# Optimization experiments

Hardware: AMD Instinct MI355X
Metric: run time of the kernel (lower is better)

Reference implementation:

```python
import jax, jax.numpy as jnp
import numpy as np

N = 100000   # total nodes (batched molecules)
E = 250000   # directed edges
B = 2000     # number of graphs
F_IN = 75    # atom feature dim
DIM = 32     # hidden dim


def setup_inputs() -> dict:
    key = jax.random.key(0)
    ks = jax.random.split(key, 12)
    def gl(k, shape, fan_in):
        return (jax.random.normal(k, shape, jnp.float32) / np.sqrt(fan_in)).astype(jnp.float32)
    inp = {}
    inp['node_features'] = jax.random.normal(ks[0], (N, F_IN), jnp.float32)
    inp['edge_features'] = jax.random.normal(ks[1], (E, 11), jnp.float32)
    inp['lin0_w'] = gl(ks[2], (DIM, F_IN), F_IN)
    inp['lin0_b'] = jnp.zeros((DIM,), jnp.float32)
    # edge network: Linear(11,128) -> ReLU -> Linear(128, DIM*DIM)
    inp['nn_w1'] = gl(ks[3], (128, 11), 11)
    inp['nn_b1'] = jnp.zeros((128,), jnp.float32)
    inp['nn_w2'] = gl(ks[4], (DIM * DIM, 128), 128)
    inp['nn_b2'] = jnp.zeros((DIM * DIM,), jnp.float32)
    inp['conv_bias'] = jnp.zeros((DIM,), jnp.float32)  # NNConv bias (root_weight=False)
    # GRU(dim, dim), torch gate order: r, z, n
    inp['gru_wih'] = gl(ks[5], (3 * DIM, DIM), DIM)
    inp['gru_whh'] = gl(ks[6], (3 * DIM, DIM), DIM)
    inp['gru_bih'] = jnp.zeros((3 * DIM,), jnp.float32)
    inp['gru_bhh'] = jnp.zeros((3 * DIM,), jnp.float32)
    # Set2Set LSTM(2*dim, dim), torch gate order: i, f, g, o
    inp['lstm_wih'] = gl(ks[7], (4 * DIM, 2 * DIM), 2 * DIM)
    inp['lstm_whh'] = gl(ks[8], (4 * DIM, DIM), DIM)
    inp['lstm_bih'] = jnp.zeros((4 * DIM,), jnp.float32)
    inp['lstm_bhh'] = jnp.zeros((4 * DIM,), jnp.float32)
    inp['edge_index'] = jax.random.randint(ks[9], (2, E), 0, N)
    inp['graph_index'] = jnp.sort(jax.random.randint(ks[10], (N,), 0, B))
    return inp


def _nnconv(x, edge_w, src, dst, bias):
    # per-edge: gather src features, apply [dim,dim] edge weight, scatter-mean to dst
    msg = jnp.einsum('ei,eio->eo', x[src], edge_w)           # [E, DIM]
    s = jax.ops.segment_sum(msg, dst, num_segments=N)         # [N, DIM]
    cnt = jax.ops.segment_sum(jnp.ones((msg.shape[0],), msg.dtype), dst, num_segments=N)
    mean = s / jnp.maximum(cnt, 1.0)[:, None]
    return mean + bias


def _gru_cell(x, h, wih, whh, bih, bhh):
    gi = x @ wih.T + bih
    gh = h @ whh.T + bhh
    gi_r, gi_z, gi_n = jnp.split(gi, 3, axis=-1)
    gh_r, gh_z, gh_n = jnp.split(gh, 3, axis=-1)
    r = jax.nn.sigmoid(gi_r + gh_r)
    z = jax.nn.sigmoid(gi_z + gh_z)
    n = jnp.tanh(gi_n + r * gh_n)
    return (1.0 - z) * n + z * h


def _lstm_cell(x, h, c, wih, whh, bih, bhh):
    g = x @ wih.T + bih + h @ whh.T + bhh
    i, f, gg, o = jnp.split(g, 4, axis=-1)
    c = jax.nn.sigmoid(f) * c + jax.nn.sigmoid(i) * jnp.tanh(gg)
    h = jax.nn.sigmoid(o) * jnp.tanh(c)
    return h, c


def _set2set(x, batch, wih, whh, bih, bhh, steps=3):
    dim = x.shape[-1]
    h = jnp.zeros((B, dim), x.dtype)
    c = jnp.zeros((B, dim), x.dtype)
    q_star = jnp.zeros((B, 2 * dim), x.dtype)
    for _ in range(steps):
        q, c = _lstm_cell(q_star, h, c, wih, whh, bih, bhh)
        h = q
        e = jnp.sum(x * q[batch], axis=-1)                    # [N]
        emax = jax.ops.segment_max(e, batch, num_segments=B)
        ex = jnp.exp(e - emax[batch])
        denom = jax.ops.segment_sum(ex, batch, num_segments=B)
        a = ex / denom[batch]
        r = jax.ops.segment_sum(a[:, None] * x, batch, num_segments=B)
        q_star = jnp.concatenate([q, r], axis=-1)
    return q_star


def reference(node_features, edge_features, lin0_w, lin0_b, nn_w1, nn_b1, nn_w2, nn_b2,
              conv_bias, gru_wih, gru_whh, gru_bih, gru_bhh,
              lstm_wih, lstm_whh, lstm_bih, lstm_bhh, edge_index, graph_index):
    src, dst = edge_index[0], edge_index[1]
    out = jax.nn.relu(node_features @ lin0_w.T + lin0_b)      # [N, DIM]
    # edge network (edge_features are fixed -> identical every iteration)
    hw = jax.nn.relu(edge_features @ nn_w1.T + nn_b1)
    edge_w = (hw @ nn_w2.T + nn_b2).reshape(-1, DIM, DIM)     # [E, DIM, DIM]
    h = out
    for _ in range(3):
        m = jax.nn.relu(_nnconv(out, edge_w, src, dst, conv_bias))
        h = _gru_cell(m, h, gru_wih, gru_whh, gru_bih, gru_bhh)
        out = h
    pooled = _set2set(out, graph_index, lstm_wih, lstm_whh, lstm_bih, lstm_bhh)
    return pooled, out
```

## Files before the change

kernel.cpp:

```cpp
#include <hip/hip_runtime.h>
#include <stdint.h>

#define N_NODES  100000
#define N_EDGES  250000
#define N_GRAPHS 2000
#define F_IN     75
#define DIM      32
#define H1       128

#define MSG_BLOCKS 977
#define CH        8
#define NSTAGES   17
#define KT_PAD    (CH * NSTAGES)
#define W2F_HALFS (KT_PAD * 1024)

typedef _Float16 v8h __attribute__((ext_vector_type(8)));
typedef float    v4f __attribute__((ext_vector_type(4)));

__device__ __forceinline__ void gld_lds16(const void* g, void* l) {
    __builtin_amdgcn_global_load_lds(
        (const __attribute__((address_space(1))) unsigned int*)g,
        (__attribute__((address_space(3))) unsigned int*)l, 16, 0, 0);
}

__global__ __launch_bounds__(256) void lin0_kernel(
    const float* __restrict__ nf, const float* __restrict__ w,
    const float* __restrict__ b, float* __restrict__ h) {
    __shared__ float wl[DIM * F_IN];
    __shared__ float bl[DIM];
    int t = threadIdx.x;
    for (int i = t; i < DIM * F_IN; i += 256) wl[i] = w[i];
    if (t < DIM) bl[t] = b[t];
    __syncthreads();
    int nl = t >> 5, o = t & 31;
    #pragma unroll
    for (int p = 0; p < 4; ++p) {
        int n = blockIdx.x * 32 + p * 8 + nl;
        if (n >= N_NODES) continue;
        const float* row = nf + (size_t)n * F_IN;
        float acc = bl[o];
        #pragma unroll
        for (int i = 0; i < F_IN; ++i) acc += row[i] * wl[o * F_IN + i];
        h[n * DIM + o] = fmaxf(acc, 0.f);
    }
}

__global__ __launch_bounds__(256) void prep_w2f_kernel(
    const float* __restrict__ w2, const float* __restrict__ b2,
    _Float16* __restrict__ w2f) {
    int id = blockIdx.x * 256 + threadIdx.x;
    if (id >= W2F_HALFS) return;
    int j    = id & 7;
    int lane = (id >> 3) & 63;
    int ng   = (id >> 9) & 1;
    int kt   = id >> 10;
    int lr = lane & 15, q = lane >> 4;
    int c = kt * 32 + q * 8 + j;
    int o = ng * 16 + lr;
    float val = 0.f;
    if (c < 4096)      val = w2[((c >> 7) * 32 + o) * H1 + (c & 127)];
    else if (c < 4128) val = b2[(c - 4096) * 32 + o];
    w2f[id] = (_Float16)val;
}

__global__ __launch_bounds__(256) void hw_kernel(
    const float* __restrict__ ef, const float* __restrict__ w1,
    const float* __restrict__ b1, _Float16* __restrict__ hwf,
    int e_off) {
    __shared__ float wl[H1 * 11];
    __shared__ float bl[H1];
    int t = threadIdx.x;
    for (int i = t; i < H1 * 11; i += 256) wl[i] = w1[i];
    if (t < H1) bl[t] = b1[t];
    __syncthreads();
    int k = t & 127;
    #pragma unroll
    for (int p = 0; p < 16; ++p) {
        int le = blockIdx.x * 32 + p * 2 + (t >> 7);
        int e  = e_off + le;
        float acc = 0.f;
        if (e < N_EDGES) {
            const float* row = ef + (size_t)e * 11;
            acc = bl[k];
            #pragma unroll
            for (int i = 0; i < 11; ++i) acc += row[i] * wl[k * 11 + i];
            acc = fmaxf(acc, 0.f);
        }
        size_t addr = (size_t)(le >> 4) * 2048 + (k >> 3) * 128 + (le & 15) * 8 + (k & 7);
        hwf[addr] = (_Float16)acc;
    }
}

__global__ __launch_bounds__(256) void cnt_kernel(
    const int* __restrict__ dst, float* __restrict__ cnt) {
    int e = blockIdx.x * 256 + threadIdx.x;
    if (e < N_EDGES) atomicAdd(&cnt[dst[e]], 1.0f);
}

__global__ __launch_bounds__(256) void offs_kernel(
    const int* __restrict__ gidx, int* __restrict__ gstart) {
    int n = blockIdx.x * 256 + threadIdx.x;
    if (n >= N_NODES) return;
    int b = gidx[n];
    if (n == 0) {
        for (int bb = 0; bb <= b; ++bb) gstart[bb] = 0;
    } else {
        int a = gidx[n - 1];
        for (int bb = a + 1; bb <= b; ++bb) gstart[bb] = n;
    }
    if (n == N_NODES - 1) {
        for (int bb = b + 1; bb <= N_GRAPHS; ++bb) gstart[bb] = N_NODES;
    }
}

__global__ __launch_bounds__(256) void msg_kernel(
    const _Float16* __restrict__ hwf, const _Float16* __restrict__ w2f,
    const float* __restrict__ x, const int* __restrict__ src,
    const int* __restrict__ dst, float* __restrict__ sbuf, int e_off) {
    __shared__ _Float16 xs[32 * 256];
    __shared__ _Float16 bst[2][CH * 1024];

    int t = threadIdx.x;
    int w = t >> 6, lane = t & 63, lr = lane & 15, q = lane >> 4;
    int wbase = w * 64;

    {
        const char* gp = (const char*)w2f;
        char* lp = (char*)&bst[0][0];
        #pragma unroll
        for (int it = 0; it < 4; ++it)
            gld_lds16(gp + it * 4096 + t * 16, lp + it * 4096 + t * 16);
    }

    v8h hwr[4][4];
    {
        const v8h* hv = (const v8h*)hwf;
        int T0 = blockIdx.x * 16 + w * 4;
        #pragma unroll
        for (int mt = 0; mt < 4; ++mt)
            #pragma unroll
            for (int kc = 0; kc < 4; ++kc)
                hwr[mt][kc] = hv[(size_t)(T0 + mt) * 256 + (kc * 4 + q) * 16 + lr];
    }

    {
        int e = e_off + blockIdx.x * 256 + t;
        int ec = e < N_EDGES ? e : N_EDGES - 1;
        int sv = src[ec];
        const float4* xr = (const float4*)(x + (size_t)sv * DIM);
        #pragma unroll
        for (int u = 0; u < 8; ++u) {
            float4 v = xr[u];
            xs[(u * 4 + 0) * 256 + t] = (_Float16)v.x;
            xs[(u * 4 + 1) * 256 + t] = (_Float16)v.y;
            xs[(u * 4 + 2) * 256 + t] = (_Float16)v.z;
            xs[(u * 4 + 3) * 256 + t] = (_Float16)v.w;
        }
    }
    __syncthreads();

    v4f acc[4][2];
    #pragma unroll
    for (int mt = 0; mt < 4; ++mt)
        #pragma unroll
        for (int ng = 0; ng < 2; ++ng) { v4f z = {0.f, 0.f, 0.f, 0.f}; acc[mt][ng] = z; }

    _Float16 xsc[4];

    for (int s = 0; s < NSTAGES - 1; ++s) {
        {
            const char* gp = (const char*)(w2f + (size_t)(s + 1) * CH * 1024);
            char* lp = (char*)&bst[(s + 1) & 1][0];
            #pragma unroll
            for (int it = 0; it < 4; ++it)
                gld_lds16(gp + it * 4096 + t * 16, lp + it * 4096 + t * 16);
        }
        const _Float16* bb = &bst[s & 1][0];
        #pragma unroll
        for (int ktl = 0; ktl < CH; ++ktl) {
            int kt = s * CH + ktl;
            v8h b0 = *(const v8h*)(bb + ktl * 1024 + lane * 8);
            v8h b1 = *(const v8h*)(bb + ktl * 1024 + 512 + lane * 8);
            if ((kt & 3) == 0) {
                int i = kt >> 2;
                #pragma unroll
                for (int mt = 0; mt < 4; ++mt)
                    xsc[mt] = xs[i * 256 + wbase + mt * 16 + lr];
            }
            int kc = kt & 3;
            #pragma unroll
            for (int mt = 0; mt < 4; ++mt) {
                v8h a = hwr[mt][kc] * xsc[mt];
                acc[mt][0] = __builtin_amdgcn_mfma_f32_16x16x32_f16(a, b0, acc[mt][0], 0, 0, 0);
                acc[mt][1] = __builtin_amdgcn_mfma_f32_16x16x32_f16(a, b1, acc[mt][1], 0, 0, 0);
            }
        }
        __syncthreads();
    }
    {
        const _Float16* bb = &bst[0][0];
        v8h b0 = *(const v8h*)(bb + lane * 8);
        v8h b1 = *(const v8h*)(bb + 512 + lane * 8);
        #pragma unroll
        for (int mt = 0; mt < 4; ++mt) {
            v8h a;
            #pragma unroll
            for (int j = 0; j < 8; ++j)
                a[j] = xs[(q * 8 + j) * 256 + wbase + mt * 16 + lr];
            acc[mt][0] = __builtin_amdgcn_mfma_f32_16x16x32_f16(a, b0, acc[mt][0], 0, 0, 0);
            acc[mt][1] = __builtin_amdgcn_mfma_f32_16x16x32_f16(a, b1, acc[mt][1], 0, 0, 0);
        }
    }

    int E0 = e_off + blockIdx.x * 256 + wbase;
    #pragma unroll
    for (int mt = 0; mt < 4; ++mt) {
        #pragma unroll
        for (int r = 0; r < 4; ++r) {
            int e = E0 + mt * 16 + q * 4 + r;
            if (e < N_EDGES) {
                int dv = dst[e];
                float* sp = sbuf + (size_t)dv * DIM;
                atomicAdd(sp + lr,      acc[mt][0][r]);
                atomicAdd(sp + 16 + lr, acc[mt][1][r]);
            }
        }
    }
}

__global__ __launch_bounds__(256) void gru_kernel(
    const float* __restrict__ s, const float* __restrict__ cnt,
    const float* __restrict__ cb,
    const float* __restrict__ wih, const float* __restrict__ whh,
    const float* __restrict__ bih, const float* __restrict__ bhh,
    float* __restrict__ h) {
    __shared__ _Float16 m_l[64 * 32];
    __shared__ _Float16 h_l[64 * 32];
    int t = threadIdx.x;

    {
        int node_l = t >> 2, part = t & 3;
        int n = blockIdx.x * 64 + node_l;
        int nc = n < N_NODES ? n : N_NODES - 1;
        float c = cnt[nc];
        float rc = 1.f / (c > 1.f ? c : 1.f);
        const float4* s4 = (const float4*)(s + (size_t)nc * DIM + part * 8);
        float4 sa = s4[0], sb = s4[1];
        const float* cbp = cb + part * 8;
        v8h mv;
        mv[0] = (_Float16)fmaxf(sa.x * rc + cbp[0], 0.f);
        mv[1] = (_Float16)fmaxf(sa.y * rc + cbp[1], 0.f);
        mv[2] = (_Float16)fmaxf(sa.z * rc + cbp[2], 0.f);
        mv[3] = (_Float16)fmaxf(sa.w * rc + cbp[3], 0.f);
        mv[4] = (_Float16)fmaxf(sb.x * rc + cbp[4], 0.f);
        mv[5] = (_Float16)fmaxf(sb.y * rc + cbp[5], 0.f);
        mv[6] = (_Float16)fmaxf(sb.z * rc + cbp[6], 0.f);
        mv[7] = (_Float16)fmaxf(sb.w * rc + cbp[7], 0.f);
        *(v8h*)&m_l[node_l * 32 + part * 8] = mv;
        const float4* h4 = (const float4*)(h + (size_t)nc * DIM + part * 8);
        float4 ha = h4[0], hb = h4[1];
        v8h hv;
        hv[0] = (_Float16)ha.x; hv[1] = (_Float16)ha.y;
        hv[2] = (_Float16)ha.z; hv[3] = (_Float16)ha.w;
        hv[4] = (_Float16)hb.x; hv[5] = (_Float16)hb.y;
        hv[6] = (_Float16)hb.z; hv[7] = (_Float16)hb.w;
        *(v8h*)&h_l[node_l * 32 + part * 8] = hv;
    }

    int w = t >> 6, lane = t & 63, lr = lane & 15, q = lane >> 4;

    v8h bi6[6], bh6[6];
    v4f ai[6], ah[6];
    #pragma unroll
    for (int nt = 0; nt < 6; ++nt) {
        const float* wr = wih + (size_t)(nt * 16 + lr) * 32 + q * 8;
        float4 wa = *(const float4*)wr, wb = *(const float4*)(wr + 4);
        v8h bv;
        bv[0] = (_Float16)wa.x; bv[1] = (_Float16)wa.y;
        bv[2] = (_Float16)wa.z; bv[3] = (_Float16)wa.w;
        bv[4] = (_Float16)wb.x; bv[5] = (_Float16)wb.y;
        bv[6] = (_Float16)wb.z; bv[7] = (_Float16)wb.w;
        bi6[nt] = bv;
        const float* wr2 = whh + (size_t)(nt * 16 + lr) * 32 + q * 8;
        float4 ha2 = *(const float4*)wr2, hb2 = *(const float4*)(wr2 + 4);
        v8h bv2;
        bv2[0] = (_Float16)ha2.x; bv2[1] = (_Float16)ha2.y;
        bv2[2] = (_Float16)ha2.z; bv2[3] = (_Float16)ha2.w;
        bv2[4] = (_Float16)hb2.x; bv2[5] = (_Float16)hb2.y;
        bv2[6] = (_Float16)hb2.z; bv2[7] = (_Float16)hb2.w;
        bh6[nt] = bv2;
        float bii = bih[nt * 16 + lr], bhi = bhh[nt * 16 + lr];
        v4f ci = {bii, bii, bii, bii}; ai[nt] = ci;
        v4f chh = {bhi, bhi, bhi, bhi}; ah[nt] = chh;
    }

    __syncthreads();

    v8h ma = *(const v8h*)&m_l[(w * 16 + lr) * 32 + q * 8];
    v8h ha = *(const v8h*)&h_l[(w * 16 + lr) * 32 + q * 8];
    #pragma unroll
    for (int nt = 0; nt < 6; ++nt) {
        ai[nt] = __builtin_amdgcn_mfma_f32_16x16x32_f16(ma, bi6[nt], ai[nt], 0, 0, 0);
        ah[nt] = __builtin_amdgcn_mfma_f32_16x16x32_f16(ha, bh6[nt], ah[nt], 0, 0, 0);
    }

    int nb = blockIdx.x * 64 + w * 16 + q * 4;
    #pragma unroll
    for (int g = 0; g < 2; ++g) {
        int o = g * 16 + lr;
        #pragma unroll
        for (int r = 0; r < 4; ++r) {
            int n2 = nb + r;
            if (n2 < N_NODES) {
                float rg = 1.f / (1.f + expf(-(ai[g][r]     + ah[g][r])));
                float zg = 1.f / (1.f + expf(-(ai[2 + g][r] + ah[2 + g][r])));
                float ng = tanhf(ai[4 + g][r] + rg * ah[4 + g][r]);
                float hold = h[(size_t)n2 * DIM + o];
                h[(size_t)n2 * DIM + o] = (1.f - zg) * ng + zg * hold;
            }
        }
    }
}

__global__ __launch_bounds__(256) void s2s_lstm_kernel(
    const float* __restrict__ wih, const float* __restrict__ whh,
    const float* __restrict__ bih, const float* __restrict__ bhh,
    float* __restrict__ h, float* __restrict__ c,
    const float* __restrict__ rnum, const float* __restrict__ denom,
    int first) {
    __shared__ float wA[128 * 33], wB[128 * 33], bl[128];
    int t = threadIdx.x;
    for (int i = t; i < 128 * 32; i += 256) {
        int r = i >> 5, cc = i & 31;
        wA[r * 33 + cc] = wih[r * 64 + cc] + whh[r * 32 + cc];
        wB[r * 33 + cc] = wih[r * 64 + 32 + cc];
    }
    if (t < 128) bl[t] = bih[t] + bhh[t];
    __syncthreads();
    int gl = t >> 5, o = t & 31;
    int b = blockIdx.x * 8 + gl;
    if (b >= N_GRAPHS) return;
    float hq = 0.f, rr = 0.f, cv = 0.f;
    if (!first) {
        hq = h[b * DIM + o];
        float d = denom[b];
        rr = d > 0.f ? rnum[b * DIM + o] / d : 0.f;
        cv = c[b * DIM + o];
    }
    float gi = bl[o], gf = bl[32 + o], gg = bl[64 + o], go = bl[96 + o];
    #pragma unroll
    for (int i = 0; i < 32; ++i) {
        float qv = __shfl(hq, i, 32);
        float rv = __shfl(rr, i, 32);
        gi += qv * wA[o * 33 + i]        + rv * wB[o * 33 + i];
        gf += qv * wA[(32 + o) * 33 + i] + rv * wB[(32 + o) * 33 + i];
        gg += qv * wA[(64 + o) * 33 + i] + rv * wB[(64 + o) * 33 + i];
        go += qv * wA[(96 + o) * 33 + i] + rv * wB[(96 + o) * 33 + i];
    }
    float si = 1.f / (1.f + expf(-gi));
    float sf = 1.f / (1.f + expf(-gf));
    float so = 1.f / (1.f + expf(-go));
    float cn = sf * cv + si * tanhf(gg);
    c[b * DIM + o] = cn;
    h[b * DIM + o] = so * tanhf(cn);
}

__global__ __launch_bounds__(256) void s2s_attn_kernel(
    const float* __restrict__ x, const float* __restrict__ q,
    const int* __restrict__ gstart,
    float* __restrict__ rnum, float* __restrict__ denom) {
    int t = threadIdx.x;
    int g = t >> 5, o = t & 31;
    int b = blockIdx.x * 8 + g;
    if (b >= N_GRAPHS) return;
    int n0 = gstart[b], n1 = gstart[b + 1];
    float qo = q[b * DIM + o];
    float m0 = -3.0e38f, s = 0.f, r = 0.f;
    for (int n = n0; n < n1; ++n) {
        float xo = x[(size_t)n * DIM + o];
        float e = xo * qo;
        #pragma unroll
        for (int mm = 16; mm >= 1; mm >>= 1) e += __shfl_xor(e, mm, 32);
        float nm = fmaxf(m0, e);
        float sc = expf(m0 - nm);
        float ex = expf(e - nm);
        s = s * sc + ex;
        r = r * sc + ex * xo;
        m0 = nm;
    }
    rnum[b * DIM + o] = r;
    if (o == 0) denom[b] = s;
}

__global__ __launch_bounds__(256) void pooled_kernel(
    const float* __restrict__ h, const float* __restrict__ rnum,
    const float* __restrict__ denom, float* __restrict__ out) {
    int t = blockIdx.x * 256 + threadIdx.x;
    int b = t >> 6, j = t & 63;
    if (b >= N_GRAPHS) return;
    float v;
    if (j < 32) v = h[b * DIM + j];
    else {
        float d = denom[b];
        v = d > 0.f ? rnum[b * DIM + (j - 32)] / d : 0.f;
    }
    out[b * 64 + j] = v;
}

extern "C" void kernel_launch(void* const* d_in, const int* in_sizes, int n_in,
                              void* d_out, int out_size, void* d_ws, size_t ws_size,
                              hipStream_t stream) {
    const float* nf   = (const float*)d_in[0];
    const float* ef   = (const float*)d_in[1];
    const float* l0w  = (const float*)d_in[2];
    const float* l0b  = (const float*)d_in[3];
    const float* w1   = (const float*)d_in[4];
    const float* b1   = (const float*)d_in[5];
    const float* w2   = (const float*)d_in[6];
    const float* b2   = (const float*)d_in[7];
    const float* cb   = (const float*)d_in[8];
    const float* gwih = (const float*)d_in[9];
    const float* gwhh = (const float*)d_in[10];
    const float* gbih = (const float*)d_in[11];
    const float* gbhh = (const float*)d_in[12];
    const float* lwih = (const float*)d_in[13];
    const float* lwhh = (const float*)d_in[14];
    const float* lbih = (const float*)d_in[15];
    const float* lbhh = (const float*)d_in[16];
    const int*   eidx = (const int*)d_in[17];
    const int*   gidx = (const int*)d_in[18];
    const int* src = eidx;
    const int* dst = eidx + N_EDGES;
    float* out = (float*)d_out;
    float* h   = out + (size_t)N_GRAPHS * 64;

    char* ws = (char*)d_ws;
    size_t off = 0;
    auto alloc = [&](size_t bytes) -> void* {
        void* p = ws + off;
        off = (off + bytes + 255) & ~(size_t)255;
        return p;
    };
    float* sbuf  = (float*)alloc((size_t)N_NODES * DIM * 4);
    float* cnt   = (float*)alloc((size_t)N_NODES * 4);
    float* hs    = (float*)alloc((size_t)N_GRAPHS * DIM * 4);
    float* cs    = (float*)alloc((size_t)N_GRAPHS * DIM * 4);
    float* rnum  = (float*)alloc((size_t)N_GRAPHS * DIM * 4);
    float* denom = (float*)alloc((size_t)N_GRAPHS * 4);
    int*   gstart = (int*)alloc((size_t)(N_GRAPHS + 1) * 4);
    _Float16* w2f  = (_Float16*)alloc((size_t)W2F_HALFS * 2);
    size_t fixed = off;
    size_t avail = ws_size > fixed ? ws_size - fixed : 0;

    auto need = [&](int nc) -> size_t {
        int cbk = (MSG_BLOCKS + nc - 1) / nc;
        return (size_t)cbk * 16 * 4096;
    };
    int nchunk = 1;
    while (nchunk < 64 && need(nchunk) > avail) nchunk <<= 1;
    int chunk_blocks = (MSG_BLOCKS + nchunk - 1) / nchunk;
    _Float16* hwf = (_Float16*)alloc(need(nchunk));

    lin0_kernel<<<dim3((N_NODES + 31) / 32), dim3(256), 0, stream>>>(nf, l0w, l0b, h);
    prep_w2f_kernel<<<dim3((W2F_HALFS + 255) / 256), dim3(256), 0, stream>>>(w2, b2, w2f);
    hipMemsetAsync(cnt, 0, (size_t)N_NODES * 4, stream);
    cnt_kernel<<<dim3((N_EDGES + 255) / 256), dim3(256), 0, stream>>>(dst, cnt);
    offs_kernel<<<dim3((N_NODES + 255) / 256), dim3(256), 0, stream>>>(gidx, gstart);
    if (nchunk == 1) {
        hw_kernel<<<dim3(MSG_BLOCKS * 8), dim3(256), 0, stream>>>(ef, w1, b1, hwf, 0);
    }

    for (int it = 0; it < 3; ++it) {
        hipMemsetAsync(sbuf, 0, (size_t)N_NODES * DIM * 4, stream);
        for (int cix = 0; cix < nchunk; ++cix) {
            int bstart = cix * chunk_blocks;
            int bc = MSG_BLOCKS - bstart;
            if (bc <= 0) break;
            if (bc > chunk_blocks) bc = chunk_blocks;
            int e_off = bstart * 256;
            if (nchunk > 1)
                hw_kernel<<<dim3(bc * 8), dim3(256), 0, stream>>>(ef, w1, b1, hwf, e_off);
            msg_kernel<<<dim3(bc), dim3(256), 0, stream>>>(hwf, w2f, h, src, dst, sbuf, e_off);
        }
        gru_kernel<<<dim3((N_NODES + 63) / 64), dim3(256), 0, stream>>>(
            sbuf, cnt, cb, gwih, gwhh, gbih, gbhh, h);
    }

    for (int st = 0; st < 3; ++st) {
        s2s_lstm_kernel<<<dim3((N_GRAPHS + 7) / 8), dim3(256), 0, stream>>>(
            lwih, lwhh, lbih, lbhh, hs, cs, rnum, denom, st == 0 ? 1 : 0);
        s2s_attn_kernel<<<dim3((N_GRAPHS + 7) / 8), dim3(256), 0, stream>>>(
            h, hs, gstart, rnum, denom);
    }
    pooled_kernel<<<dim3((N_GRAPHS * 64 + 255) / 256), dim3(256), 0, stream>>>(
        hs, rnum, denom, out);
}
```

Measured before the change: 638.6 us.

## Restage msg pipeline, zero sbuf in GRU, stage GRU weights in LDS, fuse pooling

The message kernel now uses 4-slice stages (33 stages, 32-iteration loop) so the per-stage x scalar load happens once per stage instead of behind a conditional. The per-iteration sbuf memset is dropped; the GRU kernel instead zeros each node's sum row after reading it, and also stages the GRU weights and biases in LDS as fp16 instead of loading them per lane from global memory. The final pooled kernel is removed by having the last attention pass write the output directly. This trades an extra write pass inside the GRU and finer-grained staging in the message loop for fewer launches and memsets.

After: 622.2 us. 2.6% less time.

```diff
diff --git a/kernel.cpp b/kernel.cpp
--- a/kernel.cpp
+++ b/kernel.cpp
@@ -9,8 +9,8 @@
 #define H1       128
 
 #define MSG_BLOCKS 977
-#define CH        8
-#define NSTAGES   17
+#define CH        4
+#define NSTAGES   33
 #define KT_PAD    (CH * NSTAGES)
 #define W2F_HALFS (KT_PAD * 1024)
 
@@ -127,9 +127,8 @@
     {
         const char* gp = (const char*)w2f;
         char* lp = (char*)&bst[0][0];
-        #pragma unroll
-        for (int it = 0; it < 4; ++it)
-            gld_lds16(gp + it * 4096 + t * 16, lp + it * 4096 + t * 16);
+        gld_lds16(gp + t * 16, lp + t * 16);
+        gld_lds16(gp + 4096 + t * 16, lp + 4096 + t * 16);
     }
 
     v8h hwr[4][4];
@@ -165,32 +164,25 @@
         #pragma unroll
         for (int ng = 0; ng < 2; ++ng) { v4f z = {0.f, 0.f, 0.f, 0.f}; acc[mt][ng] = z; }
 
-    _Float16 xsc[4];
-
-    for (int s = 0; s < NSTAGES - 1; ++s) {
+    for (int s = 0; s < 32; ++s) {
         {
             const char* gp = (const char*)(w2f + (size_t)(s + 1) * CH * 1024);
             char* lp = (char*)&bst[(s + 1) & 1][0];
-            #pragma unroll
-            for (int it = 0; it < 4; ++it)
-                gld_lds16(gp + it * 4096 + t * 16, lp + it * 4096 + t * 16);
-        }
+            gld_lds16(gp + t * 16, lp + t * 16);
+            gld_lds16(gp + 4096 + t * 16, lp + 4096 + t * 16);
+        }
+        _Float16 xsc[4];
+        #pragma unroll
+        for (int mt = 0; mt < 4; ++mt)
+            xsc[mt] = xs[s * 256 + wbase + mt * 16 + lr];
         const _Float16* bb = &bst[s & 1][0];
         #pragma unroll
         for (int ktl = 0; ktl < CH; ++ktl) {
-            int kt = s * CH + ktl;
             v8h b0 = *(const v8h*)(bb + ktl * 1024 + lane * 8);
             v8h b1 = *(const v8h*)(bb + ktl * 1024 + 512 + lane * 8);
-            if ((kt & 3) == 0) {
-                int i = kt >> 2;
-                #pragma unroll
-                for (int mt = 0; mt < 4; ++mt)
-                    xsc[mt] = xs[i * 256 + wbase + mt * 16 + lr];
-            }
-            int kc = kt & 3;
             #pragma unroll
             for (int mt = 0; mt < 4; ++mt) {
-                v8h a = hwr[mt][kc] * xsc[mt];
+                v8h a = hwr[mt][ktl] * xsc[mt];
                 acc[mt][0] = __builtin_amdgcn_mfma_f32_16x16x32_f16(a, b0, acc[mt][0], 0, 0, 0);
                 acc[mt][1] = __builtin_amdgcn_mfma_f32_16x16x32_f16(a, b1, acc[mt][1], 0, 0, 0);
             }
@@ -229,14 +221,22 @@
 }
 
 __global__ __launch_bounds__(256) void gru_kernel(
-    const float* __restrict__ s, const float* __restrict__ cnt,
+    float* __restrict__ s, const float* __restrict__ cnt,
     const float* __restrict__ cb,
     const float* __restrict__ wih, const float* __restrict__ whh,
     const float* __restrict__ bih, const float* __restrict__ bhh,
     float* __restrict__ h) {
-    __shared__ _Float16 m_l[64 * 32];
-    __shared__ _Float16 h_l[64 * 32];
-    int t = threadIdx.x;
+    __shared__ _Float16 wi_l[96 * 40], wh_l[96 * 40];
+    __shared__ float bi_l[96], bh_l[96];
+    __shared__ _Float16 m_l[64 * 32], h_l[64 * 32];
+    int t = threadIdx.x;
+
+    for (int i = t; i < 96 * 32; i += 256) {
+        int r = i >> 5, c2 = i & 31;
+        wi_l[r * 40 + c2] = (_Float16)wih[i];
+        wh_l[r * 40 + c2] = (_Float16)whh[i];
+    }
+    if (t < 96) { bi_l[t] = bih[t]; bh_l[t] = bhh[t]; }
 
     {
         int node_l = t >> 2, part = t & 3;
@@ -244,7 +244,7 @@
         int nc = n < N_NODES ? n : N_NODES - 1;
         float c = cnt[nc];
         float rc = 1.f / (c > 1.f ? c : 1.f);
-        const float4* s4 = (const float4*)(s + (size_t)nc * DIM + part * 8);
+        float4* s4 = (float4*)(s + (size_t)nc * DIM + part * 8);
         float4 sa = s4[0], sb = s4[1];
         const float* cbp = cb + part * 8;
         v8h mv;
@@ -257,6 +257,10 @@
         mv[6] = (_Float16)fmaxf(sb.z * rc + cbp[6], 0.f);
         mv[7] = (_Float16)fmaxf(sb.w * rc + cbp[7], 0.f);
         *(v8h*)&m_l[node_l * 32 + part * 8] = mv;
+        if (n < N_NODES) {
+            float4 z4 = {0.f, 0.f, 0.f, 0.f};
+            s4[0] = z4; s4[1] = z4;
+        }
         const float4* h4 = (const float4*)(h + (size_t)nc * DIM + part * 8);
         float4 ha = h4[0], hb = h4[1];
         v8h hv;
@@ -267,34 +271,20 @@
         *(v8h*)&h_l[node_l * 32 + part * 8] = hv;
     }
 
+    __syncthreads();
+
     int w = t >> 6, lane = t & 63, lr = lane & 15, q = lane >> 4;
 
     v8h bi6[6], bh6[6];
     v4f ai[6], ah[6];
     #pragma unroll
     for (int nt = 0; nt < 6; ++nt) {
-        const float* wr = wih + (size_t)(nt * 16 + lr) * 32 + q * 8;
-        float4 wa = *(const float4*)wr, wb = *(const float4*)(wr + 4);
-        v8h bv;
-        bv[0] = (_Float16)wa.x; bv[1] = (_Float16)wa.y;
-        bv[2] = (_Float16)wa.z; bv[3] = (_Float16)wa.w;
-        bv[4] = (_Float16)wb.x; bv[5] = (_Float16)wb.y;
-        bv[6] = (_Float16)wb.z; bv[7] = (_Float16)wb.w;
-        bi6[nt] = bv;
-        const float* wr2 = whh + (size_t)(nt * 16 + lr) * 32 + q * 8;
-        float4 ha2 = *(const float4*)wr2, hb2 = *(const float4*)(wr2 + 4);
-        v8h bv2;
-        bv2[0] = (_Float16)ha2.x; bv2[1] = (_Float16)ha2.y;
-        bv2[2] = (_Float16)ha2.z; bv2[3] = (_Float16)ha2.w;
-        bv2[4] = (_Float16)hb2.x; bv2[5] = (_Float16)hb2.y;
-        bv2[6] = (_Float16)hb2.z; bv2[7] = (_Float16)hb2.w;
-        bh6[nt] = bv2;
-        float bii = bih[nt * 16 + lr], bhi = bhh[nt * 16 + lr];
+        bi6[nt] = *(const v8h*)&wi_l[(nt * 16 + lr) * 40 + q * 8];
+        bh6[nt] = *(const v8h*)&wh_l[(nt * 16 + lr) * 40 + q * 8];
+        float bii = bi_l[nt * 16 + lr], bhi = bh_l[nt * 16 + lr];
         v4f ci = {bii, bii, bii, bii}; ai[nt] = ci;
         v4f chh = {bhi, bhi, bhi, bhi}; ah[nt] = chh;
     }
-
-    __syncthreads();
 
     v8h ma = *(const v8h*)&m_l[(w * 16 + lr) * 32 + q * 8];
     v8h ha = *(const v8h*)&h_l[(w * 16 + lr) * 32 + q * 8];
@@ -368,7 +358,8 @@
 __global__ __launch_bounds__(256) void s2s_attn_kernel(
     const float* __restrict__ x, const float* __restrict__ q,
     const int* __restrict__ gstart,
-    float* __restrict__ rnum, float* __restrict__ denom) {
+    float* __restrict__ rnum, float* __restrict__ denom,
+    float* __restrict__ outp, int wout) {
     int t = threadIdx.x;
     int g = t >> 5, o = t & 31;
     int b = blockIdx.x * 8 + g;
@@ -390,21 +381,10 @@
     }
     rnum[b * DIM + o] = r;
     if (o == 0) denom[b] = s;
-}
-
-__global__ __launch_bounds__(256) void pooled_kernel(
-    const float* __restrict__ h, const float* __restrict__ rnum,
-    const float* __restrict__ denom, float* __restrict__ out) {
-    int t = blockIdx.x * 256 + threadIdx.x;
-    int b = t >> 6, j = t & 63;
-    if (b >= N_GRAPHS) return;
-    float v;
-    if (j < 32) v = h[b * DIM + j];
-    else {
-        float d = denom[b];
-        v = d > 0.f ? rnum[b * DIM + (j - 32)] / d : 0.f;
-    }
-    out[b * 64 + j] = v;
+    if (wout) {
+        outp[b * 64 + o]      = qo;
+        outp[b * 64 + 32 + o] = s > 0.f ? r / s : 0.f;
+    }
 }
 
 extern "C" void kernel_launch(void* const* d_in, const int* in_sizes, int n_in,
@@ -469,9 +449,9 @@
     if (nchunk == 1) {
         hw_kernel<<<dim3(MSG_BLOCKS * 8), dim3(256), 0, stream>>>(ef, w1, b1, hwf, 0);
     }
+    hipMemsetAsync(sbuf, 0, (size_t)N_NODES * DIM * 4, stream);
 
     for (int it = 0; it < 3; ++it) {
-        hipMemsetAsync(sbuf, 0, (size_t)N_NODES * DIM * 4, stream);
         for (int cix = 0; cix < nchunk; ++cix) {
             int bstart = cix * chunk_blocks;
             int bc = MSG_BLOCKS - bstart;
@@ -490,8 +470,6 @@
         s2s_lstm_kernel<<<dim3((N_GRAPHS + 7) / 8), dim3(256), 0, stream>>>(
             lwih, lwhh, lbih, lbhh, hs, cs, rnum, denom, st == 0 ? 1 : 0);
         s2s_attn_kernel<<<dim3((N_GRAPHS + 7) / 8), dim3(256), 0, stream>>>(
-            h, hs, gstart, rnum, denom);
-    }
-    pooled_kernel<<<dim3((N_GRAPHS * 64 + 255) / 256), dim3(256), 0, stream>>>(
-        hs, rnum, denom, out);
-}
+            h, hs, gstart, rnum, denom, out, st == 2 ? 1 : 0);
+    }
+}
```
